# Performance work log

Hardware: AMD Instinct MI355X
Metric: run time of the kernel (lower is better)

The kernel has to match this reference:

```python
import jax, jax.numpy as jnp
import numpy as np

B, T, D_IN, D_EMB, H = 4, 2048, 1024, 1024, 16
HD = D_EMB // H  # head_dim = 64


def setup_inputs() -> dict:
    key = jax.random.key(0)
    k1, k2, k3 = jax.random.split(key, 3)
    scale_qkv = 1.0 / np.sqrt(D_IN)
    scale_o = 1.0 / np.sqrt(D_EMB)
    return {
        "x": jax.random.normal(k1, (B, T, D_IN), dtype=jnp.float32),
        "w_qkv": jax.random.normal(k2, (3 * D_EMB, D_IN), dtype=jnp.float32) * scale_qkv,
        "w_o": jax.random.normal(k3, (D_EMB, D_EMB), dtype=jnp.float32) * scale_o,
        "b_o": jnp.zeros((D_EMB,), dtype=jnp.float32),
    }


def reference(x, w_qkv, w_o, b_o):
    Bv, Tv, _ = x.shape
    # qkv projection: [B,T,3*D_EMB] -> [B,H,T,3*HD]
    qkv = jnp.einsum('btd,ed->bte', x, w_qkv)
    qkv = qkv.reshape(Bv, Tv, H, 3 * HD).transpose(0, 2, 1, 3)
    q, k, v = jnp.split(qkv, 3, axis=-1)  # each [B,H,T,HD]
    # scaled dot product with causal mask
    logits = jnp.einsum('bhqd,bhkd->bhqk', q, k) / np.sqrt(HD)
    causal = jnp.tril(jnp.ones((Tv, Tv), dtype=bool))
    logits = jnp.where(causal, logits, -jnp.inf)
    attn = jax.nn.softmax(logits, axis=-1)
    vals = jnp.einsum('bhqk,bhkd->bhqd', attn, v)
    vals = vals.transpose(0, 2, 1, 3).reshape(Bv, Tv, D_EMB)
    return jnp.einsum('bte,oe->bto', vals, w_o) + b_o
```

## Files before the change

kernel.cpp:

```cpp
#include <hip/hip_runtime.h>
#include <hip/hip_bf16.h>
#include <cstdint>
#include <cstddef>

#define B_    4
#define T_    2048
#define DIN_  1024
#define DEMB_ 1024
#define H_    16
#define HD_   64
#define M_    8192
#define NQKV_ 3072

#define QSCALE 0.18033688011112042f

typedef __bf16 bf16_t;
typedef __bf16 bf16x8 __attribute__((ext_vector_type(8)));
typedef __bf16 bf16x4 __attribute__((ext_vector_type(4)));
typedef float  f32x4  __attribute__((ext_vector_type(4)));
typedef float  f32x16 __attribute__((ext_vector_type(16)));
typedef unsigned int u32x4 __attribute__((ext_vector_type(4)));

__device__ __forceinline__ bf16_t tob(float f) {
  __hip_bfloat16 h = __float2bfloat16(f);
  return __builtin_bit_cast(bf16_t, h);
}

__device__ __forceinline__ f32x4 mfma16(bf16x8 a, bf16x8 b, f32x4 c) {
  return __builtin_amdgcn_mfma_f32_16x16x32_bf16(a, b, c, 0, 0, 0);
}
__device__ __forceinline__ f32x16 mfma32(bf16x8 a, bf16x8 b, f32x16 c) {
  return __builtin_amdgcn_mfma_f32_32x32x16_bf16(a, b, c, 0, 0, 0);
}

__device__ __forceinline__ float fexp2(float x) {
#if __has_builtin(__builtin_amdgcn_exp2f)
  return __builtin_amdgcn_exp2f(x);
#else
  return exp2f(x);
#endif
}

__device__ __forceinline__ unsigned pk2(float lo, float hi) {
  unsigned r;
  asm("v_cvt_pk_bf16_f32 %0, %1, %2" : "=v"(r) : "v"(lo), "v"(hi));
  return r;
}

__device__ __forceinline__ void plswap(unsigned& a, unsigned& b) {
  asm("v_permlane32_swap_b32 %0, %1" : "+v"(a), "+v"(b));
}

__device__ __forceinline__ void gload16(const void* g, void* l) {
  __builtin_amdgcn_global_load_lds((const __attribute__((address_space(1))) void*)g,
                                   (__attribute__((address_space(3))) void*)l, 16, 0, 0);
}

__global__ __launch_bounds__(256) void cast3_kernel(const float* __restrict__ a, bf16_t* __restrict__ ao,
                                                    const float* __restrict__ b, bf16_t* __restrict__ bo,
                                                    const float* __restrict__ c, bf16_t* __restrict__ co) {
  constexpr int na4 = M_ * DIN_ / 4;
  constexpr int nb4 = NQKV_ * DIN_ / 4;
  const int i = blockIdx.x * 256 + threadIdx.x;
  const float* src; bf16_t* dst; int off;
  if (i < na4)            { src = a; dst = ao; off = i; }
  else if (i < na4 + nb4) { src = b; dst = bo; off = i - na4; }
  else                    { src = c; dst = co; off = i - na4 - nb4; }
  float4 v = ((const float4*)src)[off];
  bf16x4 o;
  o[0] = tob(v.x); o[1] = tob(v.y); o[2] = tob(v.z); o[3] = tob(v.w);
  ((bf16x4*)dst)[off] = o;
}

__global__ __launch_bounds__(256, 3) void gemm_qkv_kernel(const bf16_t* __restrict__ A,
                                                          const bf16_t* __restrict__ Bm,
                                                          bf16_t* __restrict__ qb,
                                                          bf16_t* __restrict__ kb,
                                                          bf16_t* __restrict__ vbT) {
  constexpr int K = DIN_;
  __shared__ __align__(16) bf16_t As[128 * 64];
  __shared__ __align__(16) bf16_t Bs[128 * 64];
  const int tid = threadIdx.x, w = tid >> 6, l = tid & 63;
  const int lh = l >> 4, lr = l & 15;
  const int m0 = blockIdx.y * 128, n0 = blockIdx.x * 128;
  const int ar0 = (w >> 1) * 64, bc0 = (w & 1) * 64;
  f32x4 acc[4][4] = {};
  for (int k0 = 0; k0 < K; k0 += 64) {
#pragma unroll
    for (int i = 0; i < 4; ++i) {
      const int jx = i * 256 + tid;
      const int row = jx >> 3, us = (jx & 7) ^ (row & 7);
      gload16(A  + (size_t)(m0 + row) * K + k0 + us * 8, (char*)As + (size_t)(i * 256 + w * 64) * 16);
      gload16(Bm + (size_t)(n0 + row) * K + k0 + us * 8, (char*)Bs + (size_t)(i * 256 + w * 64) * 16);
    }
    __syncthreads();
#pragma unroll
    for (int kk = 0; kk < 2; ++kk) {
      bf16x8 af[4], bfv[4];
#pragma unroll
      for (int mi = 0; mi < 4; ++mi) {
        const int r = ar0 + mi * 16 + lr;
        af[mi] = *(const bf16x8*)&As[r * 64 + (((kk * 4 + lh) ^ (r & 7)) * 8)];
      }
#pragma unroll
      for (int ni = 0; ni < 4; ++ni) {
        const int r = bc0 + ni * 16 + lr;
        bfv[ni] = *(const bf16x8*)&Bs[r * 64 + (((kk * 4 + lh) ^ (r & 7)) * 8)];
      }
      __builtin_amdgcn_s_setprio(1);
#pragma unroll
      for (int mi = 0; mi < 4; ++mi)
#pragma unroll
        for (int ni = 0; ni < 4; ++ni)
          acc[mi][ni] = mfma16(af[mi], bfv[ni], acc[mi][ni]);
      __builtin_amdgcn_s_setprio(0);
    }
    __syncthreads();
  }
#pragma unroll
  for (int mi = 0; mi < 4; ++mi) {
    const int gm0 = m0 + ar0 + mi * 16 + lh * 4;
    const int bb = gm0 >> 11, t0 = gm0 & (T_ - 1);
#pragma unroll
    for (int ni = 0; ni < 4; ++ni) {
      const int gn = n0 + bc0 + ni * 16 + lr;
      const int h = gn / 192, s = gn - h * 192;
      const size_t bhb = (size_t)bb * H_ + h;
      if (s < 64) {
#pragma unroll
        for (int r = 0; r < 4; ++r)
          qb[(bhb * T_ + t0 + r) * HD_ + s] = tob(acc[mi][ni][r] * QSCALE);
      } else if (s < 128) {
#pragma unroll
        for (int r = 0; r < 4; ++r)
          kb[(bhb * T_ + t0 + r) * HD_ + s - 64] = tob(acc[mi][ni][r]);
      } else {
        bf16x4 pv;
#pragma unroll
        for (int r = 0; r < 4; ++r) pv[r] = tob(acc[mi][ni][r]);
        *(bf16x4*)&vbT[(bhb * HD_ + (s - 128)) * T_ + t0] = pv;
      }
    }
  }
}

__global__ __launch_bounds__(256, 2) void attn2_kernel(const bf16_t* __restrict__ qg,
                                                       const bf16_t* __restrict__ kg,
                                                       const bf16_t* __restrict__ vtg,
                                                       bf16_t* __restrict__ ob) {
  __shared__ __align__(16) bf16_t Kl[2][128 * 72];
  __shared__ __align__(16) bf16_t Vl[2][64 * 136];
  const int id = blockIdx.x;
  const int x  = (id >> 3) & 7;
  const int bh = (id & 7) | ((id >> 6) << 3);
  const int tid = threadIdx.x, w = tid >> 6, l = tid & 63;
  const int q5 = l & 31, hi = l >> 5, hi8 = hi * 8;
  const int srow = tid >> 3, scol = (tid & 7) * 8;
  const bf16_t* Qg  = qg  + (size_t)bh * T_ * HD_;
  const bf16_t* Kg  = kg  + (size_t)bh * T_ * HD_;
  const bf16_t* Vtg = vtg + (size_t)bh * HD_ * T_;

  for (int ph = 0; ph < 2; ++ph) {
    const int qt = ph ? (15 - x) : x;
    const int qb = qt * 128 + w * 32;
    const int thrD = w * 32 + q5 - 4 * hi;

    bf16x8 bq[4];
#pragma unroll
    for (int s = 0; s < 4; ++s)
      bq[s] = *(const bf16x8*)&Qg[(size_t)(qb + q5) * HD_ + s * 16 + hi8];

    f32x16 o0 = {}, o1 = {};
    float lrun = 0.f;

    {
#pragma unroll
      for (int j = 0; j < 4; ++j)
        *(bf16x8*)&Kl[0][(srow + 32 * j) * 72 + scol] =
            *(const bf16x8*)&Kg[(size_t)(srow + 32 * j) * HD_ + scol];
#pragma unroll
      for (int j = 0; j < 2; ++j)
#pragma unroll
        for (int k = 0; k < 2; ++k)
          *(bf16x8*)&Vl[0][(srow + 32 * j) * 136 + scol + 64 * k] =
              *(const bf16x8*)&Vtg[(size_t)(srow + 32 * j) * T_ + scol + 64 * k];
    }
    __syncthreads();
    int cur = 0;

    for (int kt = 0; kt <= qt; ++kt) {
      const bool more = (kt < qt);
      bf16x8 nk[4], nv[4];
      if (more) {
#pragma unroll
        for (int j = 0; j < 4; ++j)
          nk[j] = *(const bf16x8*)&Kg[(size_t)((kt + 1) * 128 + srow + 32 * j) * HD_ + scol];
#pragma unroll
        for (int j = 0; j < 2; ++j)
#pragma unroll
          for (int k = 0; k < 2; ++k)
            nv[j * 2 + k] = *(const bf16x8*)&Vtg[(size_t)(srow + 32 * j) * T_ + (kt + 1) * 128 + scol + 64 * k];
      }
      f32x16 s0 = {}, s1 = {}, s2 = {}, s3 = {};
      __builtin_amdgcn_s_setprio(1);
#pragma unroll
      for (int ss = 0; ss < 4; ++ss) {
        bf16x8 a0 = *(const bf16x8*)&Kl[cur][(q5)      * 72 + ss * 16 + hi8];
        bf16x8 a1 = *(const bf16x8*)&Kl[cur][(q5 + 32) * 72 + ss * 16 + hi8];
        bf16x8 a2 = *(const bf16x8*)&Kl[cur][(q5 + 64) * 72 + ss * 16 + hi8];
        bf16x8 a3 = *(const bf16x8*)&Kl[cur][(q5 + 96) * 72 + ss * 16 + hi8];
        s0 = mfma32(a0, bq[ss], s0);
        s1 = mfma32(a1, bq[ss], s1);
        s2 = mfma32(a2, bq[ss], s2);
        s3 = mfma32(a3, bq[ss], s3);
      }
      __builtin_amdgcn_s_setprio(0);
      if (kt == qt) {
#pragma unroll
        for (int r = 0; r < 16; ++r) {
          const int kvc = (r & 3) + 8 * (r >> 2);
          s0[r] = (kvc      > thrD) ? -1e30f : s0[r];
          s1[r] = (kvc + 32 > thrD) ? -1e30f : s1[r];
          s2[r] = (kvc + 64 > thrD) ? -1e30f : s2[r];
          s3[r] = (kvc + 96 > thrD) ? -1e30f : s3[r];
        }
      }
      float l0 = 0.f, l1 = 0.f;
#pragma unroll
      for (int r = 0; r < 16; ++r) {
        s0[r] = fexp2(s0[r]); s1[r] = fexp2(s1[r]);
        s2[r] = fexp2(s2[r]); s3[r] = fexp2(s3[r]);
        l0 += s0[r] + s1[r];
        l1 += s2[r] + s3[r];
      }
      lrun += l0 + l1;
#pragma unroll
      for (int t32 = 0; t32 < 4; ++t32) {
        const f32x16& p = (t32 == 0) ? s0 : (t32 == 1) ? s1 : (t32 == 2) ? s2 : s3;
#pragma unroll
        for (int sq = 0; sq < 2; ++sq) {
          unsigned a0 = pk2(p[8 * sq + 0], p[8 * sq + 1]);
          unsigned a1 = pk2(p[8 * sq + 2], p[8 * sq + 3]);
          unsigned b0 = pk2(p[8 * sq + 4], p[8 * sq + 5]);
          unsigned b1 = pk2(p[8 * sq + 6], p[8 * sq + 7]);
          plswap(a0, b0);
          plswap(a1, b1);
          u32x4 fw = {a0, a1, b0, b1};
          const bf16x8 pb = __builtin_bit_cast(bf16x8, fw);
          const int kvo = t32 * 32 + sq * 16 + hi8;
          bf16x8 av0 = *(const bf16x8*)&Vl[cur][(q5)      * 136 + kvo];
          bf16x8 av1 = *(const bf16x8*)&Vl[cur][(q5 + 32) * 136 + kvo];
          __builtin_amdgcn_s_setprio(1);
          o0 = mfma32(av0, pb, o0);
          o1 = mfma32(av1, pb, o1);
          __builtin_amdgcn_s_setprio(0);
        }
      }
      if (more) {
#pragma unroll
        for (int j = 0; j < 4; ++j)
          *(bf16x8*)&Kl[cur ^ 1][(srow + 32 * j) * 72 + scol] = nk[j];
#pragma unroll
        for (int j = 0; j < 2; ++j)
#pragma unroll
          for (int k = 0; k < 2; ++k)
            *(bf16x8*)&Vl[cur ^ 1][(srow + 32 * j) * 136 + scol + 64 * k] = nv[j * 2 + k];
      }
      __syncthreads();
      cur ^= 1;
    }

    const float ltot = lrun + __shfl_xor(lrun, 32);
    const float inv = 1.f / ltot;
    const size_t rowb = ((size_t)(bh >> 4) * T_ + qb + q5) * DEMB_ + (bh & 15) * HD_;
#pragma unroll
    for (int g = 0; g < 4; ++g) {
      bf16x4 st0, st1;
#pragma unroll
      for (int j = 0; j < 4; ++j) {
        st0[j] = tob(o0[4 * g + j] * inv);
        st1[j] = tob(o1[4 * g + j] * inv);
      }
      *(bf16x4*)&ob[rowb + 8 * g + 4 * hi]      = st0;
      *(bf16x4*)&ob[rowb + 8 * g + 4 * hi + 32] = st1;
    }
  }
}

__global__ __launch_bounds__(256, 3) void gemm_out_kernel(const bf16_t* __restrict__ A,
                                                          const bf16_t* __restrict__ Bm,
                                                          const float* __restrict__ bo,
                                                          float* __restrict__ out) {
  constexpr int K = DEMB_;
  __shared__ __align__(16) bf16_t As[128 * 64];
  __shared__ __align__(16) bf16_t Bs[128 * 64];
  const int tid = threadIdx.x, w = tid >> 6, l = tid & 63;
  const int lh = l >> 4, lr = l & 15;
  const int m0 = blockIdx.y * 128, n0 = blockIdx.x * 128;
  const int ar0 = (w >> 1) * 64, bc0 = (w & 1) * 64;
  f32x4 acc[4][4] = {};
  for (int k0 = 0; k0 < K; k0 += 64) {
#pragma unroll
    for (int i = 0; i < 4; ++i) {
      const int jx = i * 256 + tid;
      const int row = jx >> 3, us = (jx & 7) ^ (row & 7);
      gload16(A  + (size_t)(m0 + row) * K + k0 + us * 8, (char*)As + (size_t)(i * 256 + w * 64) * 16);
      gload16(Bm + (size_t)(n0 + row) * K + k0 + us * 8, (char*)Bs + (size_t)(i * 256 + w * 64) * 16);
    }
    __syncthreads();
#pragma unroll
    for (int kk = 0; kk < 2; ++kk) {
      bf16x8 af[4], bfv[4];
#pragma unroll
      for (int mi = 0; mi < 4; ++mi) {
        const int r = ar0 + mi * 16 + lr;
        af[mi] = *(const bf16x8*)&As[r * 64 + (((kk * 4 + lh) ^ (r & 7)) * 8)];
      }
#pragma unroll
      for (int ni = 0; ni < 4; ++ni) {
        const int r = bc0 + ni * 16 + lr;
        bfv[ni] = *(const bf16x8*)&Bs[r * 64 + (((kk * 4 + lh) ^ (r & 7)) * 8)];
      }
      __builtin_amdgcn_s_setprio(1);
#pragma unroll
      for (int mi = 0; mi < 4; ++mi)
#pragma unroll
        for (int ni = 0; ni < 4; ++ni)
          acc[mi][ni] = mfma16(af[mi], bfv[ni], acc[mi][ni]);
      __builtin_amdgcn_s_setprio(0);
    }
    __syncthreads();
  }
#pragma unroll
  for (int mi = 0; mi < 4; ++mi) {
#pragma unroll
    for (int r = 0; r < 4; ++r) {
      const int gm = m0 + ar0 + mi * 16 + lh * 4 + r;
#pragma unroll
      for (int ni = 0; ni < 4; ++ni) {
        const int gn = n0 + bc0 + ni * 16 + lr;
        out[(size_t)gm * DEMB_ + gn] = acc[mi][ni][r] + bo[gn];
      }
    }
  }
}

extern "C" void kernel_launch(void* const* d_in, const int* in_sizes, int n_in,
                              void* d_out, int out_size, void* d_ws, size_t ws_size,
                              hipStream_t stream) {
  (void)in_sizes; (void)n_in; (void)out_size; (void)ws_size;
  const float* x     = (const float*)d_in[0];
  const float* w_qkv = (const float*)d_in[1];
  const float* w_o   = (const float*)d_in[2];
  const float* b_o   = (const float*)d_in[3];
  float* out = (float*)d_out;

  char* p = (char*)d_ws;
  bf16_t* xb    = (bf16_t*)p; p += (size_t)M_ * DIN_ * 2;
  bf16_t* wqkvb = (bf16_t*)p; p += (size_t)NQKV_ * DIN_ * 2;
  bf16_t* wob   = (bf16_t*)p; p += (size_t)DEMB_ * DEMB_ * 2;
  bf16_t* qbuf  = (bf16_t*)p; p += (size_t)B_ * H_ * T_ * HD_ * 2;
  bf16_t* kbuf  = (bf16_t*)p; p += (size_t)B_ * H_ * T_ * HD_ * 2;
  bf16_t* vbuf  = (bf16_t*)p; p += (size_t)B_ * H_ * T_ * HD_ * 2;
  bf16_t* attnb = xb;

  constexpr int CAST_BLOCKS = (M_ * DIN_ + NQKV_ * DIN_ + DEMB_ * DEMB_) / 1024;
  cast3_kernel<<<CAST_BLOCKS, 256, 0, stream>>>(x, xb, w_qkv, wqkvb, w_o, wob);
  gemm_qkv_kernel<<<dim3(NQKV_ / 128, M_ / 128), 256, 0, stream>>>(xb, wqkvb, qbuf, kbuf, vbuf);
  attn2_kernel<<<512, 256, 0, stream>>>(qbuf, kbuf, vbuf, attnb);
  gemm_out_kernel<<<dim3(DEMB_ / 128, M_ / 128), 256, 0, stream>>>(attnb, wob, b_o, out);
}
```

Before: 153.0 us.

## Double-buffer LDS tiles in QKV and output GEMMs with async prefetch

Both projection GEMMs now keep two LDS buffers per operand and prefetch the k-tile two steps ahead with global_load_lds. Partial vmcnt waits and raw barriers replace __syncthreads, so global loads overlap with MFMA work instead of stalling every iteration. In exchange, LDS use per block doubles, which lowers the occupancy target from 3 to 2 blocks per CU. This relies on manual waitcnt accounting of 8 outstanding loads per stage.

```diff
diff --git a/kernel.cpp b/kernel.cpp
--- a/kernel.cpp
+++ b/kernel.cpp
@@ -54,6 +54,14 @@
 __device__ __forceinline__ void gload16(const void* g, void* l) {
   __builtin_amdgcn_global_load_lds((const __attribute__((address_space(1))) void*)g,
                                    (__attribute__((address_space(3))) void*)l, 16, 0, 0);
+}
+
+__device__ __forceinline__ void wait_vm8()  { asm volatile("s_waitcnt vmcnt(8)" ::: "memory"); }
+__device__ __forceinline__ void wait_vm0()  { asm volatile("s_waitcnt vmcnt(0)" ::: "memory"); }
+__device__ __forceinline__ void raw_bar() {
+  __builtin_amdgcn_sched_barrier(0);
+  __builtin_amdgcn_s_barrier();
+  __builtin_amdgcn_sched_barrier(0);
 }
 
 __global__ __launch_bounds__(256) void cast3_kernel(const float* __restrict__ a, bf16_t* __restrict__ ao,
@@ -72,40 +80,51 @@
   ((bf16x4*)dst)[off] = o;
 }
 
-__global__ __launch_bounds__(256, 3) void gemm_qkv_kernel(const bf16_t* __restrict__ A,
+__global__ __launch_bounds__(256, 2) void gemm_qkv_kernel(const bf16_t* __restrict__ A,
                                                           const bf16_t* __restrict__ Bm,
                                                           bf16_t* __restrict__ qb,
                                                           bf16_t* __restrict__ kb,
                                                           bf16_t* __restrict__ vbT) {
   constexpr int K = DIN_;
-  __shared__ __align__(16) bf16_t As[128 * 64];
-  __shared__ __align__(16) bf16_t Bs[128 * 64];
+  constexpr int NT = K / 64;
+  __shared__ __align__(16) bf16_t As[2][128 * 64];
+  __shared__ __align__(16) bf16_t Bs[2][128 * 64];
   const int tid = threadIdx.x, w = tid >> 6, l = tid & 63;
   const int lh = l >> 4, lr = l & 15;
   const int m0 = blockIdx.y * 128, n0 = blockIdx.x * 128;
   const int ar0 = (w >> 1) * 64, bc0 = (w & 1) * 64;
-  f32x4 acc[4][4] = {};
-  for (int k0 = 0; k0 < K; k0 += 64) {
+
+  auto stage = [&](int kt, int buf) {
 #pragma unroll
     for (int i = 0; i < 4; ++i) {
       const int jx = i * 256 + tid;
       const int row = jx >> 3, us = (jx & 7) ^ (row & 7);
-      gload16(A  + (size_t)(m0 + row) * K + k0 + us * 8, (char*)As + (size_t)(i * 256 + w * 64) * 16);
-      gload16(Bm + (size_t)(n0 + row) * K + k0 + us * 8, (char*)Bs + (size_t)(i * 256 + w * 64) * 16);
-    }
-    __syncthreads();
+      gload16(A  + (size_t)(m0 + row) * K + kt * 64 + us * 8,
+              (char*)&As[buf][0] + (size_t)(i * 256 + w * 64) * 16);
+      gload16(Bm + (size_t)(n0 + row) * K + kt * 64 + us * 8,
+              (char*)&Bs[buf][0] + (size_t)(i * 256 + w * 64) * 16);
+    }
+  };
+
+  f32x4 acc[4][4] = {};
+  stage(0, 0);
+  stage(1, 1);
+  for (int kt = 0; kt < NT; ++kt) {
+    const int cur = kt & 1;
+    if (kt + 1 < NT) wait_vm8(); else wait_vm0();
+    raw_bar();
 #pragma unroll
     for (int kk = 0; kk < 2; ++kk) {
       bf16x8 af[4], bfv[4];
 #pragma unroll
       for (int mi = 0; mi < 4; ++mi) {
         const int r = ar0 + mi * 16 + lr;
-        af[mi] = *(const bf16x8*)&As[r * 64 + (((kk * 4 + lh) ^ (r & 7)) * 8)];
+        af[mi] = *(const bf16x8*)&As[cur][r * 64 + (((kk * 4 + lh) ^ (r & 7)) * 8)];
       }
 #pragma unroll
       for (int ni = 0; ni < 4; ++ni) {
         const int r = bc0 + ni * 16 + lr;
-        bfv[ni] = *(const bf16x8*)&Bs[r * 64 + (((kk * 4 + lh) ^ (r & 7)) * 8)];
+        bfv[ni] = *(const bf16x8*)&Bs[cur][r * 64 + (((kk * 4 + lh) ^ (r & 7)) * 8)];
       }
       __builtin_amdgcn_s_setprio(1);
 #pragma unroll
@@ -115,7 +134,8 @@
           acc[mi][ni] = mfma16(af[mi], bfv[ni], acc[mi][ni]);
       __builtin_amdgcn_s_setprio(0);
     }
-    __syncthreads();
+    raw_bar();
+    if (kt + 2 < NT) stage(kt + 2, cur);
   }
 #pragma unroll
   for (int mi = 0; mi < 4; ++mi) {
@@ -287,39 +307,50 @@
   }
 }
 
-__global__ __launch_bounds__(256, 3) void gemm_out_kernel(const bf16_t* __restrict__ A,
+__global__ __launch_bounds__(256, 2) void gemm_out_kernel(const bf16_t* __restrict__ A,
                                                           const bf16_t* __restrict__ Bm,
                                                           const float* __restrict__ bo,
                                                           float* __restrict__ out) {
   constexpr int K = DEMB_;
-  __shared__ __align__(16) bf16_t As[128 * 64];
-  __shared__ __align__(16) bf16_t Bs[128 * 64];
+  constexpr int NT = K / 64;
+  __shared__ __align__(16) bf16_t As[2][128 * 64];
+  __shared__ __align__(16) bf16_t Bs[2][128 * 64];
   const int tid = threadIdx.x, w = tid >> 6, l = tid & 63;
   const int lh = l >> 4, lr = l & 15;
   const int m0 = blockIdx.y * 128, n0 = blockIdx.x * 128;
   const int ar0 = (w >> 1) * 64, bc0 = (w & 1) * 64;
-  f32x4 acc[4][4] = {};
-  for (int k0 = 0; k0 < K; k0 += 64) {
+
+  auto stage = [&](int kt, int buf) {
 #pragma unroll
     for (int i = 0; i < 4; ++i) {
       const int jx = i * 256 + tid;
       const int row = jx >> 3, us = (jx & 7) ^ (row & 7);
-      gload16(A  + (size_t)(m0 + row) * K + k0 + us * 8, (char*)As + (size_t)(i * 256 + w * 64) * 16);
-      gload16(Bm + (size_t)(n0 + row) * K + k0 + us * 8, (char*)Bs + (size_t)(i * 256 + w * 64) * 16);
-    }
-    __syncthreads();
+      gload16(A  + (size_t)(m0 + row) * K + kt * 64 + us * 8,
+              (char*)&As[buf][0] + (size_t)(i * 256 + w * 64) * 16);
+      gload16(Bm + (size_t)(n0 + row) * K + kt * 64 + us * 8,
+              (char*)&Bs[buf][0] + (size_t)(i * 256 + w * 64) * 16);
+    }
+  };
+
+  f32x4 acc[4][4] = {};
+  stage(0, 0);
+  stage(1, 1);
+  for (int kt = 0; kt < NT; ++kt) {
+    const int cur = kt & 1;
+    if (kt + 1 < NT) wait_vm8(); else wait_vm0();
+    raw_bar();
 #pragma unroll
     for (int kk = 0; kk < 2; ++kk) {
       bf16x8 af[4], bfv[4];
 #pragma unroll
       for (int mi = 0; mi < 4; ++mi) {
         const int r = ar0 + mi * 16 + lr;
-        af[mi] = *(const bf16x8*)&As[r * 64 + (((kk * 4 + lh) ^ (r & 7)) * 8)];
+        af[mi] = *(const bf16x8*)&As[cur][r * 64 + (((kk * 4 + lh) ^ (r & 7)) * 8)];
       }
 #pragma unroll
       for (int ni = 0; ni < 4; ++ni) {
         const int r = bc0 + ni * 16 + lr;
-        bfv[ni] = *(const bf16x8*)&Bs[r * 64 + (((kk * 4 + lh) ^ (r & 7)) * 8)];
+        bfv[ni] = *(const bf16x8*)&Bs[cur][r * 64 + (((kk * 4 + lh) ^ (r & 7)) * 8)];
       }
       __builtin_amdgcn_s_setprio(1);
 #pragma unroll
@@ -329,7 +360,8 @@
           acc[mi][ni] = mfma16(af[mi], bfv[ni], acc[mi][ni]);
       __builtin_amdgcn_s_setprio(0);
     }
-    __syncthreads();
+    raw_bar();
+    if (kt + 2 < NT) stage(kt + 2, cur);
   }
 #pragma unroll
   for (int mi = 0; mi < 4; ++mi) {
```

After: 158.3 us. 3.5% more time.
